# Performance work log

Hardware: AMD Instinct MI355X
Metric: run time of the kernel (lower is better)

## Reference

```python
import jax, jax.numpy as jnp
import numpy as np

S = 1024          # tokens (prefill)
DIM = 2560
HEAD_DIM = 128
N_HEADS = 20
N_KV = 5
HPG = N_HEADS // N_KV      # heads per kv group = 4
GS = 128                   # weight-scale group size
THETA = 500000.0
EPS = 1e-05
QKV_OUT = (N_HEADS + 2 * N_KV) * HEAD_DIM  # 3840


def setup_inputs() -> dict:
    key = jax.random.key(0)
    ks = jax.random.split(key, 7)
    x = jax.random.normal(ks[0], (S, DIM), jnp.float32)
    # unpacked int2 (ternary) weights, stored as float for the reference math
    w_qkv = jax.random.randint(ks[1], (QKV_OUT, DIM), -1, 2).astype(jnp.float32)
    ws_qkv = jax.random.uniform(ks[2], (QKV_OUT, DIM // GS), jnp.float32, 0.01, 0.05)
    w_o = jax.random.randint(ks[3], (DIM, N_HEADS * HEAD_DIM), -1, 2).astype(jnp.float32)
    ws_o = jax.random.uniform(ks[4], (DIM, N_HEADS * HEAD_DIM // GS), jnp.float32, 0.01, 0.05)
    q_norm_w = 1.0 + 0.02 * jax.random.normal(ks[5], (HEAD_DIM,), jnp.float32)
    k_norm_w = 1.0 + 0.02 * jax.random.normal(ks[6], (HEAD_DIM,), jnp.float32)
    return {"x": x, "w_qkv": w_qkv, "ws_qkv": ws_qkv, "w_o": w_o, "ws_o": ws_o,
            "q_norm_w": q_norm_w, "k_norm_w": k_norm_w}


def _quant_act(x):
    # per-token symmetric int8 quant: s = 127 / max|x| (clamped)
    s = 127.0 / jnp.clip(jnp.max(jnp.abs(x), axis=-1, keepdims=True), 1e-05, None)
    q = jnp.clip(jnp.round(x * s), -128.0, 127.0)
    return q, s


def _bitlinear(x, w, ws):
    # int8 activation x int2 weight GEMM with per-(out,group) dequant scales
    q, s = _quant_act(x)
    w_dq = w * jnp.repeat(ws, GS, axis=1)        # [out, in]
    return (q @ w_dq.T) / s


def _rmsnorm(x, w):
    return x * jax.lax.rsqrt(jnp.mean(x * x, axis=-1, keepdims=True) + EPS) * w


def _rope(x, cos, sin):
    # x: [S, ..., d]; cos/sin: [S, d//2], interleaved-pair (llama) convention
    d2 = x.shape[-1] // 2
    shape = (x.shape[0],) + (1,) * (x.ndim - 2) + (d2,)
    c = cos.reshape(shape)
    s = sin.reshape(shape)
    xr = x.reshape(x.shape[:-1] + (d2, 2))
    x0, x1 = xr[..., 0], xr[..., 1]
    out = jnp.stack([x0 * c - x1 * s, x0 * s + x1 * c], axis=-1)
    return out.reshape(x.shape)


def reference(x, w_qkv, ws_qkv, w_o, ws_o, q_norm_w, k_norm_w):
    qkv = _bitlinear(x, w_qkv, ws_qkv)                       # [S, 3840]
    q_size = N_HEADS * HEAD_DIM
    k_size = N_KV * HEAD_DIM
    xq = qkv[:, :q_size].reshape(S, N_KV, HPG, HEAD_DIM)     # [S, g, h, d]
    xk = qkv[:, q_size:q_size + k_size].reshape(S, N_KV, HEAD_DIM)
    xv = qkv[:, q_size + k_size:].reshape(S, N_KV, HEAD_DIM)
    xq = _rmsnorm(xq, q_norm_w)
    xk = _rmsnorm(xk, k_norm_w)
    # RoPE (prefill: positions 0..S-1)
    pos = jnp.arange(S, dtype=jnp.float32)
    inv_freq = THETA ** (-jnp.arange(0, HEAD_DIM, 2, dtype=jnp.float32) / HEAD_DIM)
    ang = pos[:, None] * inv_freq[None, :]                   # [S, d/2]
    cos, sin = jnp.cos(ang), jnp.sin(ang)
    xq = _rope(xq, cos, sin)
    xk = _rope(xk, cos, sin)
    # GQA causal flash-attention math
    scale = HEAD_DIM ** -0.5
    scores = jnp.einsum('sghd,tgd->ghst', xq, xk) * scale    # [g, h, S, S]
    causal = jnp.tril(jnp.ones((S, S), bool))
    scores = jnp.where(causal, scores, -1e30)
    attn = jax.nn.softmax(scores, axis=-1)
    out = jnp.einsum('ghst,tgd->sghd', attn, xv).reshape(S, N_HEADS * HEAD_DIM)
    return _bitlinear(out, w_o, ws_o)                        # [S, DIM]
```

## Files before the change

kernel.cpp:

```cpp
#include <hip/hip_runtime.h>
#include <hip/hip_bf16.h>
#include <cstdint>
#include <math.h>

#define SEQ 1024
#define DIM 2560
#define HD 128
#define NH 20
#define NKV 5
#define QKV_OUT 3840
#define GS 128

typedef __bf16 bf16;
typedef __bf16 bf16x4 __attribute__((ext_vector_type(4)));
typedef __bf16 bf16x8 __attribute__((ext_vector_type(8)));
typedef float f32x4 __attribute__((ext_vector_type(4)));

template <typename T>
__global__ __launch_bounds__(256) void quant_kernel(
    const T* __restrict__ x, bf16* __restrict__ act,
    float* __restrict__ rs, int cols) {
  const int row = blockIdx.x;
  const int tid = threadIdx.x;
  const T* xr = x + (size_t)row * cols;
  float m = 0.f;
  for (int i = tid; i < cols; i += 256) m = fmaxf(m, fabsf((float)xr[i]));
  for (int off = 32; off; off >>= 1) m = fmaxf(m, __shfl_xor(m, off));
  __shared__ float red[4];
  __shared__ float s_bc;
  if ((tid & 63) == 0) red[tid >> 6] = m;
  __syncthreads();
  if (tid == 0) {
    float mm = fmaxf(fmaxf(red[0], red[1]), fmaxf(red[2], red[3]));
    mm = fmaxf(mm, 1e-5f);
    s_bc = 127.f / mm;
    rs[row] = mm / 127.f;
  }
  __syncthreads();
  const float s = s_bc;
  bf16* ar = act + (size_t)row * cols;
  for (int i = tid; i < cols; i += 256) {
    float q = rintf((float)xr[i] * s);
    q = fminf(fmaxf(q, -128.f), 127.f);
    ar[i] = (bf16)q;
  }
}

__global__ __launch_bounds__(256) void fused_pre(
    const float* __restrict__ x, bf16* __restrict__ act, float* __restrict__ rs,
    const float* __restrict__ w1, const float* __restrict__ ws1, bf16* __restrict__ o1,
    const float* __restrict__ w2, const float* __restrict__ ws2, bf16* __restrict__ o2,
    long n1_4, long total4) {
  const int tid = threadIdx.x;
  if (blockIdx.x < SEQ) {
    const int row = blockIdx.x;
    const float* xr = x + (size_t)row * DIM;
    float m = 0.f;
    for (int i = tid; i < DIM; i += 256) m = fmaxf(m, fabsf(xr[i]));
    for (int off = 32; off; off >>= 1) m = fmaxf(m, __shfl_xor(m, off));
    __shared__ float red[4];
    __shared__ float s_bc;
    if ((tid & 63) == 0) red[tid >> 6] = m;
    __syncthreads();
    if (tid == 0) {
      float mm = fmaxf(fmaxf(red[0], red[1]), fmaxf(red[2], red[3]));
      mm = fmaxf(mm, 1e-5f);
      s_bc = 127.f / mm;
      rs[row] = mm / 127.f;
    }
    __syncthreads();
    const float s = s_bc;
    bf16* ar = act + (size_t)row * DIM;
    for (int i = tid; i < DIM; i += 256) {
      float q = rintf(xr[i] * s);
      q = fminf(fmaxf(q, -128.f), 127.f);
      ar[i] = (bf16)q;
    }
  } else {
    long i = (long)(blockIdx.x - SEQ) * 256 + tid;
    if (i >= total4) return;
    const float* w; const float* ws; bf16* o; long e;
    if (i < n1_4) { w = w1; ws = ws1; o = o1; e = i * 4; }
    else          { w = w2; ws = ws2; o = o2; e = (i - n1_4) * 4; }
    int row = (int)(e / DIM);
    int k = (int)(e % DIM);
    float sc = ws[(size_t)row * (DIM / GS) + (k / GS)];
    float4 wv = *(const float4*)(w + e);
    bf16x4 ov;
    ov[0] = (bf16)(wv.x * sc);
    ov[1] = (bf16)(wv.y * sc);
    ov[2] = (bf16)(wv.z * sc);
    ov[3] = (bf16)(wv.w * sc);
    *(bf16x4*)(o + e) = ov;
  }
}

__device__ __forceinline__ void gload_lds16(const bf16* g, bf16* l) {
  __builtin_amdgcn_global_load_lds(
      (const __attribute__((address_space(1))) void*)g,
      (__attribute__((address_space(3))) void*)l, 16, 0, 0);
}

template <int BM, int BN>
__global__ __launch_bounds__(256) void gemm_pipe(
    const bf16* __restrict__ A, const bf16* __restrict__ B,
    const float* __restrict__ rs, float* __restrict__ C,
    int N, int K, int Kh, size_t part_stride, int ND, int NN) {
  constexpr int MI = BM / 32;
  constexpr int NW = BN / 32;
  constexpr int APASS = BM / 32;
  constexpr int BPASS = BN / 32;
  __shared__ bf16 As[2][BM * 64];
  __shared__ bf16 Bs[2][BN * 64];
  const int b = (int)blockIdx.x;
  const int mtile = b / ND;
  const int nz = b % ND;
  const int ntile = nz % NN;
  const int z = nz / NN;
  const int tid = threadIdx.x;
  const int w = tid >> 6, l = tid & 63;
  const int row0 = mtile * BM;
  const int col0 = ntile * BN;
  const int wm = (w >> 1) * (BM / 2), wn = (w & 1) * (BN / 2);
  const int lcol = l & 15, quad = l >> 4;
  const int sr = l >> 3, sg = l & 7;
  const bf16* Ag = A + (size_t)row0 * K + (size_t)z * Kh;
  const bf16* Bg = B + (size_t)col0 * K + (size_t)z * Kh;

  f32x4 acc[MI][NW] = {};

#define STAGE_AB(buf, k0)                                                      \
  {                                                                            \
    _Pragma("unroll") for (int i = 0; i < APASS; ++i) {                        \
      int rb = w * (BM / 4) + i * 8;                                           \
      int r = rb + sr;                                                         \
      gload_lds16(Ag + (size_t)r * K + (k0) + ((sg ^ (r & 7)) * 8),            \
                  &As[buf][rb * 64]);                                          \
    }                                                                          \
    _Pragma("unroll") for (int i = 0; i < BPASS; ++i) {                        \
      int rb = w * (BN / 4) + i * 8;                                           \
      int r = rb + sr;                                                         \
      gload_lds16(Bg + (size_t)r * K + (k0) + ((sg ^ (r & 7)) * 8),            \
                  &Bs[buf][rb * 64]);                                          \
    }                                                                          \
  }

  STAGE_AB(0, 0)
  __syncthreads();

  int buf = 0;
  for (int k0 = 0; k0 < Kh; k0 += 64) {
    if (k0 + 64 < Kh) STAGE_AB(buf ^ 1, k0 + 64)
#pragma unroll
    for (int ks = 0; ks < 2; ++ks) {
      bf16x8 af[MI], bff[NW];
#pragma unroll
      for (int mi = 0; mi < MI; ++mi) {
        int R = wm + mi * 16 + lcol;
        af[mi] = *(const bf16x8*)(&As[buf][R * 64 + (((ks * 4 + quad) ^ (R & 7)) * 8)]);
      }
#pragma unroll
      for (int ni = 0; ni < NW; ++ni) {
        int R = wn + ni * 16 + lcol;
        bff[ni] = *(const bf16x8*)(&Bs[buf][R * 64 + (((ks * 4 + quad) ^ (R & 7)) * 8)]);
      }
#pragma unroll
      for (int mi = 0; mi < MI; ++mi)
#pragma unroll
        for (int ni = 0; ni < NW; ++ni)
          acc[mi][ni] = __builtin_amdgcn_mfma_f32_16x16x32_bf16(
              af[mi], bff[ni], acc[mi][ni], 0, 0, 0);
    }
    __syncthreads();
    buf ^= 1;
  }
#undef STAGE_AB

  float* Cp = C + (size_t)z * part_stride;
#pragma unroll
  for (int mi = 0; mi < MI; ++mi) {
#pragma unroll
    for (int ni = 0; ni < NW; ++ni) {
      int col = col0 + wn + ni * 16 + lcol;
#pragma unroll
      for (int r = 0; r < 4; ++r) {
        int row = row0 + wm + mi * 16 + quad * 4 + r;
        Cp[(size_t)row * N + col] = acc[mi][ni][r] * rs[row];
      }
    }
  }
}

__global__ __launch_bounds__(256) void fused_post(
    const float* __restrict__ qkvA, const float* __restrict__ qkvB,
    const float* __restrict__ qw, const float* __restrict__ kw,
    bf16* __restrict__ Qo, bf16* __restrict__ Ko, bf16* __restrict__ Vt) {
  __shared__ bf16 Ls[64 * 137];
  const int bx = (int)blockIdx.x;
  const int tid = threadIdx.x;
  if (bx < 6400) {
    const int wave = tid >> 6, i = tid & 63;
    const int u = bx * 4 + wave;
    const int t = u & 1023, h = u >> 10;
    const size_t off = (h < NH)
        ? (size_t)t * QKV_OUT + h * HD
        : (size_t)t * QKV_OUT + 2560 + (h - NH) * HD;
    const float* s1 = qkvA + off;
    const float* s2 = qkvB + off;
    float x0 = s1[2 * i] + s2[2 * i];
    float x1 = s1[2 * i + 1] + s2[2 * i + 1];
    float ss = x0 * x0 + x1 * x1;
    for (int off2 = 1; off2 < 64; off2 <<= 1) ss += __shfl_xor(ss, off2);
    float r = rsqrtf(ss * (1.f / 128.f) + 1e-5f);
    const float* wv = (h < NH) ? qw : kw;
    float y0 = x0 * r * wv[2 * i];
    float y1 = x1 * r * wv[2 * i + 1];
    float inv_freq = powf(500000.f, -(float)(2 * i) * (1.f / 128.f));
    float ang = (float)t * inv_freq;
    float sn, cs;
    sincosf(ang, &sn, &cs);
    float o0 = y0 * cs - y1 * sn;
    float o1 = y0 * sn + y1 * cs;
    if (h < NH) {
      bf16* dst = Qo + ((size_t)t * NH + h) * HD + 2 * i;
      dst[0] = (bf16)o0; dst[1] = (bf16)o1;
    } else {
      bf16* dst = Ko + ((size_t)(h - NH) * SEQ + t) * HD + 2 * i;
      dst[0] = (bf16)o0; dst[1] = (bf16)o1;
    }
  } else {
    const int b2 = bx - 6400;
    const int t0 = (b2 & 15) * 64, g = b2 >> 4;
    {
      const int tl = tid >> 4;
      const int d0 = (tid & 15) * 8;
#pragma unroll
      for (int pass = 0; pass < 4; ++pass) {
        int t = pass * 16 + tl;
        size_t off = (size_t)(t0 + t) * QKV_OUT + 3200 + g * HD + d0;
        float4 a = *(const float4*)(qkvA + off);
        float4 b = *(const float4*)(qkvA + off + 4);
        float4 a2 = *(const float4*)(qkvB + off);
        float4 b2v = *(const float4*)(qkvB + off + 4);
        bf16* dst = Ls + t * 137 + d0;
        dst[0] = (bf16)(a.x + a2.x); dst[1] = (bf16)(a.y + a2.y);
        dst[2] = (bf16)(a.z + a2.z); dst[3] = (bf16)(a.w + a2.w);
        dst[4] = (bf16)(b.x + b2v.x); dst[5] = (bf16)(b.y + b2v.y);
        dst[6] = (bf16)(b.z + b2v.z); dst[7] = (bf16)(b.w + b2v.w);
      }
    }
    __syncthreads();
    {
      const int dl = tid >> 3;
      const int tl0 = (tid & 7) * 8;
#pragma unroll
      for (int pass = 0; pass < 4; ++pass) {
        int d = pass * 32 + dl;
        bf16x8 v;
#pragma unroll
        for (int j = 0; j < 8; ++j) v[j] = Ls[(tl0 + j) * 137 + d];
        *(bf16x8*)(Vt + ((size_t)g * HD + d) * SEQ + t0 + tl0) = v;
      }
    }
  }
}

__global__ __launch_bounds__(256, 1) void attn_mfma(
    const bf16* __restrict__ Qb, const bf16* __restrict__ Kb,
    const bf16* __restrict__ Vt, bf16* __restrict__ O) {
  const int qb = 31 - (int)blockIdx.x;
  const int hp = blockIdx.y;
  const int tid = threadIdx.x;
  const int wave = tid >> 6, lane = tid & 63;
  const int H = (hp >> 1) * 4 + (hp & 1) * 2 + (wave >> 1);
  const int g = H >> 2;
  const int qcol = lane & 15, quad = lane >> 4;
  const int q_tok = qb * 32 + (wave & 1) * 16 + qcol;
  const float scale = 0.08838834764831843f;

  __shared__ bf16 Ks[2][64 * 128];
  __shared__ bf16 Vs[2][128 * 64];

  const bf16* kbase = Kb + (size_t)g * SEQ * HD;
  const bf16* vbase = Vt + (size_t)g * HD * SEQ;

  bf16x8 qf[4];
  {
    const bf16* qp = Qb + ((size_t)q_tok * NH + H) * HD + quad * 8;
#pragma unroll
    for (int kc = 0; kc < 4; ++kc) qf[kc] = *(const bf16x8*)(qp + kc * 32);
  }

  float m_i = -1e30f, l_i = 0.f;
  f32x4 o_acc[8] = {};
  const int kt_max = (qb * 32 + 31) >> 6;

  const int k_r = lane >> 4, k_g = lane & 15;
  const int v_r = lane >> 3, v_g = lane & 7;

#define STAGE(buf, key0)                                                       \
  {                                                                            \
    _Pragma("unroll") for (int p = 0; p < 4; ++p) {                            \
      int r0 = wave * 16 + p * 4;                                              \
      int r = r0 + k_r;                                                        \
      gload_lds16(kbase + (size_t)((key0) + r) * HD + ((k_g ^ (r & 15)) * 8),  \
                  &Ks[buf][r0 * 128]);                                         \
    }                                                                          \
    _Pragma("unroll") for (int p = 0; p < 4; ++p) {                            \
      int r0 = wave * 32 + p * 8;                                              \
      int r = r0 + v_r;                                                        \
      gload_lds16(vbase + (size_t)r * SEQ + (key0) + ((v_g ^ (r & 7)) * 8),    \
                  &Vs[buf][r0 * 64]);                                          \
    }                                                                          \
  }

  STAGE(0, 0)

  for (int kt = 0; kt <= kt_max; ++kt) {
    const int key0 = kt * 64;
    __syncthreads();
    if (kt < kt_max) STAGE((kt + 1) & 1, key0 + 64)
    const bf16* Kt = Ks[kt & 1];
    const bf16* Vtile = Vs[kt & 1];

    bf16x8 kf[4][4];
#pragma unroll
    for (int mg = 0; mg < 4; ++mg) {
      const int R = mg * 16 + qcol;
      const bf16* krow = Kt + R * 128;
#pragma unroll
      for (int kc = 0; kc < 4; ++kc)
        kf[mg][kc] = *(const bf16x8*)(krow + (((kc * 4 + quad) ^ (R & 15)) * 8));
    }
    f32x4 s[4];
#pragma unroll
    for (int mg = 0; mg < 4; ++mg) {
      f32x4 acc = {0.f, 0.f, 0.f, 0.f};
#pragma unroll
      for (int kc = 0; kc < 4; ++kc)
        acc = __builtin_amdgcn_mfma_f32_16x16x32_bf16(kf[mg][kc], qf[kc], acc, 0, 0, 0);
      s[mg] = acc;
    }

    bf16x8 vf[8][2];
#pragma unroll
    for (int mg2 = 0; mg2 < 8; ++mg2) {
      const int R = mg2 * 16 + qcol;
      const bf16* vrow = Vtile + R * 64;
#pragma unroll
      for (int c = 0; c < 2; ++c) {
        int g8a = c * 8 + quad;
        int g8b = c * 8 + 4 + quad;
        bf16x4 v0 = *(const bf16x4*)(vrow + ((g8a >> 1) ^ (R & 7)) * 8 + (g8a & 1) * 4);
        bf16x4 v1 = *(const bf16x4*)(vrow + ((g8b >> 1) ^ (R & 7)) * 8 + (g8b & 1) * 4);
#pragma unroll
        for (int j = 0; j < 4; ++j) { vf[mg2][c][j] = v0[j]; vf[mg2][c][j + 4] = v1[j]; }
      }
    }

    float mt = -1e30f;
#pragma unroll
    for (int mg = 0; mg < 4; ++mg)
#pragma unroll
      for (int r = 0; r < 4; ++r) {
        int key = key0 + mg * 16 + quad * 4 + r;
        float v = (key <= q_tok) ? s[mg][r] * scale : -1e30f;
        s[mg][r] = v;
        mt = fmaxf(mt, v);
      }
    mt = fmaxf(mt, __shfl_xor(mt, 16));
    mt = fmaxf(mt, __shfl_xor(mt, 32));
    float mnew = fmaxf(m_i, mt);
    float alpha = __expf(m_i - mnew);
    float ps = 0.f;
#pragma unroll
    for (int mg = 0; mg < 4; ++mg)
#pragma unroll
      for (int r = 0; r < 4; ++r) {
        float pv = __expf(s[mg][r] - mnew);
        s[mg][r] = pv;
        ps += pv;
      }
    ps += __shfl_xor(ps, 16);
    ps += __shfl_xor(ps, 32);
    l_i = l_i * alpha + ps;
    m_i = mnew;
#pragma unroll
    for (int mg2 = 0; mg2 < 8; ++mg2)
#pragma unroll
      for (int r = 0; r < 4; ++r) o_acc[mg2][r] *= alpha;

    bf16x8 pb[2];
#pragma unroll
    for (int c = 0; c < 2; ++c)
#pragma unroll
      for (int j = 0; j < 8; ++j)
        pb[c][j] = (bf16)s[c * 2 + (j >> 2)][j & 3];

#pragma unroll
    for (int mg2 = 0; mg2 < 8; ++mg2) {
      f32x4 acc = o_acc[mg2];
#pragma unroll
      for (int c = 0; c < 2; ++c)
        acc = __builtin_amdgcn_mfma_f32_16x16x32_bf16(vf[mg2][c], pb[c], acc, 0, 0, 0);
      o_acc[mg2] = acc;
    }
  }
#undef STAGE

  const float inv = 1.f / l_i;
  bf16* op = O + (size_t)q_tok * DIM + H * HD + quad * 4;
#pragma unroll
  for (int mg2 = 0; mg2 < 8; ++mg2) {
    bf16x4 vv;
    vv[0] = (bf16)(o_acc[mg2][0] * inv);
    vv[1] = (bf16)(o_acc[mg2][1] * inv);
    vv[2] = (bf16)(o_acc[mg2][2] * inv);
    vv[3] = (bf16)(o_acc[mg2][3] * inv);
    *(bf16x4*)(op + mg2 * 16) = vv;
  }
}

extern "C" void kernel_launch(void* const* d_in, const int* in_sizes, int n_in,
                              void* d_out, int out_size, void* d_ws, size_t ws_size,
                              hipStream_t stream) {
  const float* x      = (const float*)d_in[0];
  const float* w_qkv  = (const float*)d_in[1];
  const float* ws_qkv = (const float*)d_in[2];
  const float* w_o    = (const float*)d_in[3];
  const float* ws_o   = (const float*)d_in[4];
  const float* qnw    = (const float*)d_in[5];
  const float* knw    = (const float*)d_in[6];
  float* out = (float*)d_out;

  char* p = (char*)d_ws;
  bf16*  act1 = (bf16*)p;  p += (size_t)SEQ * DIM * 2;
  float* rs1  = (float*)p; p += 4096;
  bf16*  wqdq = (bf16*)p;  p += (size_t)QKV_OUT * DIM * 2;
  bf16*  wodq = (bf16*)p;  p += (size_t)DIM * DIM * 2;
  float* qkvA = (float*)p; p += (size_t)SEQ * QKV_OUT * 4;
  float* qkvB = (float*)p; p += (size_t)SEQ * QKV_OUT * 4;
  bf16*  Qb   = (bf16*)p;  p += (size_t)SEQ * NH * HD * 2;
  bf16*  Kb   = (bf16*)p;  p += (size_t)NKV * SEQ * HD * 2;
  bf16*  Vt   = (bf16*)p;  p += (size_t)NKV * HD * SEQ * 2;
  bf16*  attn = (bf16*)p;  p += (size_t)SEQ * DIM * 2;
  bf16*  act2 = (bf16*)p;  p += (size_t)SEQ * DIM * 2;
  float* rs2  = (float*)p; p += 4096;

  {
    long n1_4 = (long)QKV_OUT * DIM / 4;
    long total4 = n1_4 + (long)DIM * DIM / 4;
    int dq_blocks = (int)((total4 + 255) / 256);
    fused_pre<<<SEQ + dq_blocks, 256, 0, stream>>>(
        x, act1, rs1, w_qkv, ws_qkv, wqdq, w_o, ws_o, wodq, n1_4, total4);
  }
  gemm_pipe<128, 128><<<480, 256, 0, stream>>>(
      act1, wqdq, rs1, qkvA, QKV_OUT, DIM, DIM / 2, (size_t)SEQ * QKV_OUT, 60, 30);
  fused_post<<<6480, 256, 0, stream>>>(qkvA, qkvB, qnw, knw, Qb, Kb, Vt);
  attn_mfma<<<dim3(32, 10), 256, 0, stream>>>(Qb, Kb, Vt, attn);
  quant_kernel<bf16><<<SEQ, 256, 0, stream>>>(attn, act2, rs2, DIM);
  gemm_pipe<64, 64><<<640, 256, 0, stream>>>(
      act2, wodq, rs2, out, DIM, DIM, DIM, 0, 40, 40);
}
```

Measured before the change: 232.3 us.

## Split causal attention over key chunks and fuse merge with activation quantization

Attention blocks now process at most six key tiles each; long query blocks are split into up to three chunks to balance causal work across a larger grid. Each chunk writes unnormalized fp32 partial outputs plus running max and sum. A new merge kernel combines the chunks with log-sum-exp weights and directly performs per-token int8 quantization, replacing the separate quant pass. This costs extra fp32 partial-output traffic through reused workspace buffers.

```diff
diff --git a/kernel.cpp b/kernel.cpp
--- a/kernel.cpp
+++ b/kernel.cpp
@@ -15,36 +15,6 @@
 typedef __bf16 bf16x4 __attribute__((ext_vector_type(4)));
 typedef __bf16 bf16x8 __attribute__((ext_vector_type(8)));
 typedef float f32x4 __attribute__((ext_vector_type(4)));
-
-template <typename T>
-__global__ __launch_bounds__(256) void quant_kernel(
-    const T* __restrict__ x, bf16* __restrict__ act,
-    float* __restrict__ rs, int cols) {
-  const int row = blockIdx.x;
-  const int tid = threadIdx.x;
-  const T* xr = x + (size_t)row * cols;
-  float m = 0.f;
-  for (int i = tid; i < cols; i += 256) m = fmaxf(m, fabsf((float)xr[i]));
-  for (int off = 32; off; off >>= 1) m = fmaxf(m, __shfl_xor(m, off));
-  __shared__ float red[4];
-  __shared__ float s_bc;
-  if ((tid & 63) == 0) red[tid >> 6] = m;
-  __syncthreads();
-  if (tid == 0) {
-    float mm = fmaxf(fmaxf(red[0], red[1]), fmaxf(red[2], red[3]));
-    mm = fmaxf(mm, 1e-5f);
-    s_bc = 127.f / mm;
-    rs[row] = mm / 127.f;
-  }
-  __syncthreads();
-  const float s = s_bc;
-  bf16* ar = act + (size_t)row * cols;
-  for (int i = tid; i < cols; i += 256) {
-    float q = rintf((float)xr[i] * s);
-    q = fminf(fmaxf(q, -128.f), 127.f);
-    ar[i] = (bf16)q;
-  }
-}
 
 __global__ __launch_bounds__(256) void fused_pre(
     const float* __restrict__ x, bf16* __restrict__ act, float* __restrict__ rs,
@@ -267,8 +237,13 @@
 
 __global__ __launch_bounds__(256, 1) void attn_mfma(
     const bf16* __restrict__ Qb, const bf16* __restrict__ Kb,
-    const bf16* __restrict__ Vt, bf16* __restrict__ O) {
-  const int qb = 31 - (int)blockIdx.x;
+    const bf16* __restrict__ Vt, float* __restrict__ Op,
+    float* __restrict__ ml) {
+  const int p = (int)blockIdx.x;
+  int qb, c;
+  if (p < 24)      { qb = 31 - p / 3;            c = p % 3; }
+  else if (p < 48) { int r = p - 24; qb = 23 - (r >> 1); c = r & 1; }
+  else             { qb = 59 - p;                c = 0; }
   const int hp = blockIdx.y;
   const int tid = threadIdx.x;
   const int wave = tid >> 6, lane = tid & 63;
@@ -293,30 +268,35 @@
 
   float m_i = -1e30f, l_i = 0.f;
   f32x4 o_acc[8] = {};
-  const int kt_max = (qb * 32 + 31) >> 6;
+  const int kt0 = c * 6;
+  int kt_max = kt0 + 5;
+  {
+    int ktg = (qb * 32 + 31) >> 6;
+    if (ktg < kt_max) kt_max = ktg;
+  }
 
   const int k_r = lane >> 4, k_g = lane & 15;
   const int v_r = lane >> 3, v_g = lane & 7;
 
 #define STAGE(buf, key0)                                                       \
   {                                                                            \
-    _Pragma("unroll") for (int p = 0; p < 4; ++p) {                            \
-      int r0 = wave * 16 + p * 4;                                              \
+    _Pragma("unroll") for (int p2 = 0; p2 < 4; ++p2) {                         \
+      int r0 = wave * 16 + p2 * 4;                                             \
       int r = r0 + k_r;                                                        \
       gload_lds16(kbase + (size_t)((key0) + r) * HD + ((k_g ^ (r & 15)) * 8),  \
                   &Ks[buf][r0 * 128]);                                         \
     }                                                                          \
-    _Pragma("unroll") for (int p = 0; p < 4; ++p) {                            \
-      int r0 = wave * 32 + p * 8;                                              \
+    _Pragma("unroll") for (int p2 = 0; p2 < 4; ++p2) {                         \
+      int r0 = wave * 32 + p2 * 8;                                             \
       int r = r0 + v_r;                                                        \
       gload_lds16(vbase + (size_t)r * SEQ + (key0) + ((v_g ^ (r & 7)) * 8),    \
                   &Vs[buf][r0 * 64]);                                          \
     }                                                                          \
   }
 
-  STAGE(0, 0)
-
-  for (int kt = 0; kt <= kt_max; ++kt) {
+  STAGE(0, kt0 * 64)
+
+  for (int kt = kt0; kt <= kt_max; ++kt) {
     const int key0 = kt * 64;
     __syncthreads();
     if (kt < kt_max) STAGE((kt + 1) & 1, key0 + 64)
@@ -348,13 +328,13 @@
       const int R = mg2 * 16 + qcol;
       const bf16* vrow = Vtile + R * 64;
 #pragma unroll
-      for (int c = 0; c < 2; ++c) {
-        int g8a = c * 8 + quad;
-        int g8b = c * 8 + 4 + quad;
+      for (int cc = 0; cc < 2; ++cc) {
+        int g8a = cc * 8 + quad;
+        int g8b = cc * 8 + 4 + quad;
         bf16x4 v0 = *(const bf16x4*)(vrow + ((g8a >> 1) ^ (R & 7)) * 8 + (g8a & 1) * 4);
         bf16x4 v1 = *(const bf16x4*)(vrow + ((g8b >> 1) ^ (R & 7)) * 8 + (g8b & 1) * 4);
 #pragma unroll
-        for (int j = 0; j < 4; ++j) { vf[mg2][c][j] = v0[j]; vf[mg2][c][j + 4] = v1[j]; }
+        for (int j = 0; j < 4; ++j) { vf[mg2][cc][j] = v0[j]; vf[mg2][cc][j + 4] = v1[j]; }
       }
     }
 
@@ -392,32 +372,91 @@
 
     bf16x8 pb[2];
 #pragma unroll
-    for (int c = 0; c < 2; ++c)
+    for (int cc = 0; cc < 2; ++cc)
 #pragma unroll
       for (int j = 0; j < 8; ++j)
-        pb[c][j] = (bf16)s[c * 2 + (j >> 2)][j & 3];
+        pb[cc][j] = (bf16)s[cc * 2 + (j >> 2)][j & 3];
 
 #pragma unroll
     for (int mg2 = 0; mg2 < 8; ++mg2) {
       f32x4 acc = o_acc[mg2];
 #pragma unroll
-      for (int c = 0; c < 2; ++c)
-        acc = __builtin_amdgcn_mfma_f32_16x16x32_bf16(vf[mg2][c], pb[c], acc, 0, 0, 0);
+      for (int cc = 0; cc < 2; ++cc)
+        acc = __builtin_amdgcn_mfma_f32_16x16x32_bf16(vf[mg2][cc], pb[cc], acc, 0, 0, 0);
       o_acc[mg2] = acc;
     }
   }
 #undef STAGE
 
-  const float inv = 1.f / l_i;
-  bf16* op = O + (size_t)q_tok * DIM + H * HD + quad * 4;
-#pragma unroll
-  for (int mg2 = 0; mg2 < 8; ++mg2) {
-    bf16x4 vv;
-    vv[0] = (bf16)(o_acc[mg2][0] * inv);
-    vv[1] = (bf16)(o_acc[mg2][1] * inv);
-    vv[2] = (bf16)(o_acc[mg2][2] * inv);
-    vv[3] = (bf16)(o_acc[mg2][3] * inv);
-    *(bf16x4*)(op + mg2 * 16) = vv;
+  float* op = Op + ((size_t)c * SEQ + q_tok) * DIM + (size_t)H * HD + quad * 4;
+#pragma unroll
+  for (int mg2 = 0; mg2 < 8; ++mg2)
+    *(f32x4*)(op + mg2 * 16) = o_acc[mg2];
+  if (lane < 16) {
+    size_t mloff = (((size_t)c * SEQ + q_tok) * NH + H) * 2;
+    ml[mloff] = m_i;
+    ml[mloff + 1] = l_i;
+  }
+}
+
+__global__ __launch_bounds__(256) void merge_quant(
+    const float* __restrict__ Op, const float* __restrict__ ml,
+    bf16* __restrict__ act, float* __restrict__ rs) {
+  const int t = blockIdx.x;
+  const int tid = threadIdx.x;
+  const int nc = (((t | 31) >> 6) / 6) + 1;
+  __shared__ float sw[3][NH];
+  __shared__ float red[4];
+  __shared__ float s_bc;
+  if (tid < NH) {
+    const size_t base = ((size_t)t * NH + tid) * 2;
+    const size_t cs = (size_t)SEQ * NH * 2;
+    float m0 = ml[base], l0 = ml[base + 1];
+    float m1 = 0.f, l1 = 0.f, m2 = 0.f, l2 = 0.f;
+    float M = m0;
+    if (nc > 1) { m1 = ml[base + cs];     l1 = ml[base + cs + 1];     M = fmaxf(M, m1); }
+    if (nc > 2) { m2 = ml[base + 2 * cs]; l2 = ml[base + 2 * cs + 1]; M = fmaxf(M, m2); }
+    float w0 = __expf(m0 - M), w1 = 0.f, w2 = 0.f;
+    float L = w0 * l0;
+    if (nc > 1) { w1 = __expf(m1 - M); L += w1 * l1; }
+    if (nc > 2) { w2 = __expf(m2 - M); L += w2 * l2; }
+    const float invL = 1.f / L;
+    sw[0][tid] = w0 * invL;
+    sw[1][tid] = w1 * invL;
+    sw[2][tid] = w2 * invL;
+  }
+  __syncthreads();
+  float vals[10];
+  float amax = 0.f;
+  const float* ob = Op + (size_t)t * DIM;
+  const size_t cs = (size_t)SEQ * DIM;
+#pragma unroll
+  for (int j = 0; j < 10; ++j) {
+    int d = j * 256 + tid;
+    int h = d >> 7;
+    float v = ob[d] * sw[0][h];
+    if (nc > 1) v += ob[d + cs] * sw[1][h];
+    if (nc > 2) v += ob[d + 2 * cs] * sw[2][h];
+    vals[j] = v;
+    amax = fmaxf(amax, fabsf(v));
+  }
+  for (int off = 32; off; off >>= 1) amax = fmaxf(amax, __shfl_xor(amax, off));
+  if ((tid & 63) == 0) red[tid >> 6] = amax;
+  __syncthreads();
+  if (tid == 0) {
+    float mm = fmaxf(fmaxf(red[0], red[1]), fmaxf(red[2], red[3]));
+    mm = fmaxf(mm, 1e-5f);
+    s_bc = 127.f / mm;
+    rs[t] = mm / 127.f;
+  }
+  __syncthreads();
+  const float s = s_bc;
+  bf16* ar = act + (size_t)t * DIM;
+#pragma unroll
+  for (int j = 0; j < 10; ++j) {
+    float q = rintf(vals[j] * s);
+    q = fminf(fmaxf(q, -128.f), 127.f);
+    ar[j * 256 + tid] = (bf16)q;
   }
 }
 
@@ -443,9 +482,11 @@
   bf16*  Qb   = (bf16*)p;  p += (size_t)SEQ * NH * HD * 2;
   bf16*  Kb   = (bf16*)p;  p += (size_t)NKV * SEQ * HD * 2;
   bf16*  Vt   = (bf16*)p;  p += (size_t)NKV * HD * SEQ * 2;
-  bf16*  attn = (bf16*)p;  p += (size_t)SEQ * DIM * 2;
   bf16*  act2 = (bf16*)p;  p += (size_t)SEQ * DIM * 2;
   float* rs2  = (float*)p; p += 4096;
+
+  float* Opart = qkvA;
+  float* mlbuf = (float*)act1;
 
   {
     long n1_4 = (long)QKV_OUT * DIM / 4;
@@ -457,8 +498,8 @@
   gemm_pipe<128, 128><<<480, 256, 0, stream>>>(
       act1, wqdq, rs1, qkvA, QKV_OUT, DIM, DIM / 2, (size_t)SEQ * QKV_OUT, 60, 30);
   fused_post<<<6480, 256, 0, stream>>>(qkvA, qkvB, qnw, knw, Qb, Kb, Vt);
-  attn_mfma<<<dim3(32, 10), 256, 0, stream>>>(Qb, Kb, Vt, attn);
-  quant_kernel<bf16><<<SEQ, 256, 0, stream>>>(attn, act2, rs2, DIM);
+  attn_mfma<<<dim3(60, 10), 256, 0, stream>>>(Qb, Kb, Vt, Opart, mlbuf);
+  merge_quant<<<SEQ, 256, 0, stream>>>(Opart, mlbuf, act2, rs2);
   gemm_pipe<64, 64><<<640, 256, 0, stream>>>(
       act2, wodq, rs2, out, DIM, DIM, DIM, 0, 40, 40);
 }
```

After: 226.1 us. 1.03x faster.
